# Kernel tuning notes

Hardware: AMD Instinct MI355X
Metric: run time of the kernel (lower is better)

The kernel has to match this reference:

```python
import jax, jax.numpy as jnp
import numpy as np

DEPTH = 2
DIM = 512
FF = 2048
INNER = 32
VOCAB = 8192
B = 2
L = 512
LN_EPS = 1e-5


def _layer_norm(x, g, b):
    m = jnp.mean(x, axis=-1, keepdims=True)
    v = jnp.var(x, axis=-1, keepdims=True)
    return (x - m) * jax.lax.rsqrt(v + LN_EPS) * g + b


def _sioconv_layer(x, wa, wx, v_re, v_im, h0_re, h0_im, w_ol):
    # x: [B, L, DIM] float32
    Bb, Ll, _ = x.shape
    I = v_re.shape[0]
    # complex gate a with magnitude sigmoid(log|a|^2)
    af = (x @ wa.T).reshape(Bb, Ll, I, 2)
    a = jax.lax.complex(af[..., 0], af[..., 1])
    m = jnp.square(af[..., 0]) + jnp.square(af[..., 1])
    a = a * jax.lax.rsqrt(m) * jax.nn.sigmoid(jnp.log(m))  # [B,L,I] complex
    # complex input x with magnitude |x| (x * rsqrt(|x|^2) * |x|^2)
    xf = (x @ wx.T).reshape(Bb, Ll, I, 2)
    xc = jax.lax.complex(xf[..., 0], xf[..., 1])
    mx = jnp.square(xf[..., 0]) + jnp.square(xf[..., 1])
    xc = xc * jax.lax.rsqrt(mx) * mx  # [B,L,I] complex
    # cumulative log-decay products: the original's FFT conv of the upper-
    # triangular a_ln against an all-ones matrix is exactly a cumsum along j.
    a_ln = jnp.log(a)  # [B,L,I]
    ii = jnp.arange(Ll)[:, None]
    jj = jnp.arange(Ll)[None, :]
    tri = jnp.where((jj >= ii)[None, None, :, :],
                    jnp.transpose(a_ln, (0, 2, 1))[:, :, None, :],
                    jnp.zeros((), a_ln.dtype))  # [B,I,L,L]: tri[b,d,i,j]=a_ln[b,j,d] for j>=i
    s = jnp.cumsum(tri, axis=3)
    # c[b,d,i,j] = prod_{t=i..j} a[b,t,d] for j>=i; =1 at j=i-1; 0 below.
    c = jnp.where((jj >= ii - 1)[None, None, :, :], jnp.exp(s), jnp.zeros((), s.dtype))
    V = jax.lax.complex(v_re, v_im)
    Vinv = jnp.linalg.inv(V)
    h0 = jax.lax.complex(h0_re, h0_im)  # [I]
    xct = jnp.transpose(xc, (0, 2, 1))  # [B,I,L]
    x_roll = jnp.roll(xct, 1, axis=2).at[:, :, 0].set(h0[None, :])
    # original builds C[b,l,m,n,o] = V diag(c) V^-1 then einsum; contract lazily:
    y = jnp.einsum('ko,bol->bkl', Vinv, x_roll)  # eigenbasis inputs [B,I,L]
    t = jnp.einsum('bkij,bki->bjk', c, y)        # recurrence in eigenbasis [B,L,I]
    h = jnp.einsum('bjk,nk->bjn', t, V)          # back to state basis [B,L,I]
    h = h.at[:, -1, :].add(xc[:, -1, :])         # last step input (others already in c via j=i-1 band)
    return jnp.real(h) @ w_ol.T


def setup_inputs() -> dict:
    key = jax.random.key(0)
    ks = jax.random.split(key, 16)
    f = lambda k, shp: jax.random.normal(k, shp, dtype=jnp.float32)
    return {
        'x': f(ks[0], (B, L, VOCAB)),
        'w_in': f(ks[1], (DIM, VOCAB)) * VOCAB ** -0.5,
        'b_in': jnp.zeros((DIM,), jnp.float32),
        'ln1_g': jnp.ones((DEPTH, DIM), jnp.float32),
        'ln1_b': jnp.zeros((DEPTH, DIM), jnp.float32),
        'wa': f(ks[2], (DEPTH, 2 * INNER, DIM)) * DIM ** -0.5,
        'wx': f(ks[3], (DEPTH, 2 * INNER, DIM)) * DIM ** -0.5,
        'v_re': f(ks[4], (DEPTH, INNER, INNER)),
        'v_im': f(ks[5], (DEPTH, INNER, INNER)),
        'h0_re': f(ks[6], (DEPTH, INNER)),
        'h0_im': f(ks[7], (DEPTH, INNER)),
        'w_ol': f(ks[8], (DEPTH, DIM, INNER)) * INNER ** -0.5,
        'ln2_g': jnp.ones((DEPTH, DIM), jnp.float32),
        'ln2_b': jnp.zeros((DEPTH, DIM), jnp.float32),
        'w1': f(ks[9], (DEPTH, FF, DIM)) * DIM ** -0.5,
        'b1': jnp.zeros((DEPTH, FF), jnp.float32),
        'w2': f(ks[10], (DEPTH, DIM, FF)) * FF ** -0.5,
        'b2': jnp.zeros((DEPTH, DIM), jnp.float32),
        'lnl_g': jnp.ones((DIM,), jnp.float32),
        'lnl_b': jnp.zeros((DIM,), jnp.float32),
        'w_out': f(ks[11], (VOCAB, DIM)) * DIM ** -0.5,
        'b_out': jnp.zeros((VOCAB,), jnp.float32),
    }


def reference(x, w_in, b_in, ln1_g, ln1_b, wa, wx, v_re, v_im, h0_re, h0_im,
              w_ol, ln2_g, ln2_b, w1, b1, w2, b2, lnl_g, lnl_b, w_out, b_out):
    h = x @ w_in.T + b_in  # [B,L,DIM]
    for d in range(DEPTH):
        r = h
        z = _layer_norm(h, ln1_g[d], ln1_b[d])
        z = _sioconv_layer(z, wa[d], wx[d], v_re[d], v_im[d], h0_re[d], h0_im[d], w_ol[d])
        h = z + r
        r = h
        z = _layer_norm(h, ln2_g[d], ln2_b[d])
        z = jax.nn.silu(z @ w1[d].T + b1[d]) @ w2[d].T + b2[d]
        h = z + r
    h = _layer_norm(h, lnl_g, lnl_b)
    return h @ w_out.T + b_out
```

## Files before the change

### kernel.cpp

```cpp
#include <hip/hip_runtime.h>
#include <stdint.h>

#define DEPTHC 2
#define DIMC   512
#define FFC    2048
#define INNERC 32
#define VOCABC 8192
#define BC     2
#define LC     512
#define NTOK   1024

typedef _Float16 f16;
typedef __attribute__((ext_vector_type(8))) _Float16 f16x8;
typedef __attribute__((ext_vector_type(4))) float f32x4;

__device__ __forceinline__ float2 cmul2(float2 a, float2 b){
    return make_float2(a.x*b.x - a.y*b.y, a.x*b.y + a.y*b.x);
}
__device__ __forceinline__ float2 cadd2(float2 a, float2 b){
    return make_float2(a.x + b.x, a.y + b.y);
}

__device__ __forceinline__ void gl_lds16(const void* g, void* l){
    __builtin_amdgcn_global_load_lds(
        (const __attribute__((address_space(1))) unsigned int*)g,
        (__attribute__((address_space(3))) unsigned int*)l, 16, 0, 0);
}

__global__ __launch_bounds__(256) void k_prep(
    const float* __restrict__ s0, const float* __restrict__ s1,
    const float* __restrict__ s2, const float* __restrict__ s3,
    const float* __restrict__ s4,
    const float* __restrict__ wa4, const float* __restrict__ wx4,
    f16* __restrict__ d0, f16* __restrict__ d1, f16* __restrict__ d2,
    f16* __restrict__ d3, f16* __restrict__ d4, f16* __restrict__ wgb,
    int n0, int n1, int n2, int n3, int n4,
    const float* __restrict__ v_re, const float* __restrict__ v_im,
    const float* __restrict__ h0re, const float* __restrict__ h0im,
    float2* __restrict__ vinv, float2* __restrict__ h0c)
{
    __shared__ float2 M[32][64];
    if (blockIdx.x < 2){
        const int d = blockIdx.x;
        const int tid = threadIdx.x;
        const int c = tid & 63;
        const int wv = tid >> 6;
        if (tid < 32) h0c[d*32 + tid] = make_float2(h0re[d*32 + tid], h0im[d*32 + tid]);
#pragma unroll
        for (int rr = 0; rr < 8; ++rr){
            int r = wv*8 + rr;
            float re, im;
            if (c < 32){ re = v_re[d*1024 + r*32 + c]; im = v_im[d*1024 + r*32 + c]; }
            else       { re = (c - 32 == r) ? 1.f : 0.f; im = 0.f; }
            M[r][c] = make_float2(re, im);
        }
        __syncthreads();
#pragma unroll 1
        for (int col = 0; col < 32; ++col){
            float2 prow = M[col][c];
            float pvx = __shfl(prow.x, col, 64);
            float pvy = __shfl(prow.y, col, 64);
            float dm = pvx*pvx + pvy*pvy;
            float ir = pvx/dm, ii = -pvy/dm;
            float2 nv = make_float2(prow.x*ir - prow.y*ii, prow.x*ii + prow.y*ir);
#pragma unroll
            for (int rr = 0; rr < 8; ++rr){
                int r = wv*8 + rr;
                if (r == col) continue;
                float2 f  = M[r][col];
                float2 m0 = M[r][c];
                m0.x -= f.x*nv.x - f.y*nv.y;
                m0.y -= f.x*nv.y + f.y*nv.x;
                M[r][c] = m0;
            }
            __syncthreads();
        }
        if (c >= 32){
#pragma unroll
            for (int rr = 0; rr < 8; ++rr){
                int r = wv*8 + rr;
                float2 dv = M[r][r];
                float dm = dv.x*dv.x + dv.y*dv.y;
                float ir = dv.x/dm, ii = -dv.y/dm;
                float2 m0 = M[r][c];
                vinv[d*1024 + r*32 + (c - 32)] =
                    make_float2(m0.x*ir - m0.y*ii, m0.x*ii + m0.y*ir);
            }
        }
        return;
    }
    long long i = ((long long)(blockIdx.x - 2) * 256 + threadIdx.x) * 4;
    const float* s; f16* d;
    if (i < n0){ s = s0; d = d0; }
    else { i -= n0;
        if (i < n1){ s = s1; d = d1; }
        else { i -= n1;
            if (i < n2){ s = s2; d = d2; }
            else { i -= n2;
                if (i < n3){ s = s3; d = d3; }
                else { i -= n3;
                    if (i < n4){ s = s4; d = d4; }
                    else {
                        i -= n4;
                        if (i >= 131072) return;
                        const float* gs; f16* gd;
                        if (i < 65536){
                            int dd = (int)(i >> 15), rem = (int)(i & 32767);
                            gs = wa4 + i; gd = wgb + dd*65536 + rem;
                        } else {
                            long long e2 = i - 65536;
                            int dd = (int)(e2 >> 15), rem = (int)(e2 & 32767);
                            gs = wx4 + e2; gd = wgb + dd*65536 + 32768 + rem;
                        }
                        float4 v = *(const float4*)gs;
                        union { f16 h[4]; float2 f2; } u;
                        u.h[0] = (f16)v.x; u.h[1] = (f16)v.y; u.h[2] = (f16)v.z; u.h[3] = (f16)v.w;
                        *(float2*)gd = u.f2;
                        return;
                    }
                }
            }
        }
    }
    float4 v = *(const float4*)(s + i);
    union { f16 h[4]; float2 f2; } u;
    u.h[0] = (f16)v.x; u.h[1] = (f16)v.y; u.h[2] = (f16)v.z; u.h[3] = (f16)v.w;
    *(float2*)(d + i) = u.f2;
}

template<int MT, int NT, int MODE>
__global__ __launch_bounds__(256) void k_gemmT(
    const f16* __restrict__ A, const f16* __restrict__ Bw,
    void* __restrict__ C, const float* __restrict__ bias,
    int N, int K, int klen, int partStride,
    float2* __restrict__ a_tp, float2* __restrict__ xcp)
{
    constexpr int RM = MT/32, RN = NT/32;
    __shared__ __align__(16) f16 As[MT*64];
    __shared__ __align__(16) f16 Bs[NT*64];
    const int tid = threadIdx.x;
    const int m0 = blockIdx.y * MT;
    const int n0 = blockIdx.x * NT;
    const int kbeg = blockIdx.z * klen;
    const int l = tid & 63;
    const int w = tid >> 6;
    const int fr = l & 15;
    const int fq = l >> 4;
    const int wm = (w >> 1) * (MT/2);
    const int wn = (w & 1) * (NT/2);
    const f16* gA = A  + (size_t)(m0 + (tid >> 3)) * K + kbeg + (tid & 7) * 8;
    const f16* gB = Bw + (size_t)(n0 + (tid >> 3)) * K + kbeg + (tid & 7) * 8;
    const size_t rowskip = (size_t)32 * K;
    f16* lA = As + tid * 8;
    f16* lB = Bs + tid * 8;
    f32x4 acc[RM][RN];
#pragma unroll
    for (int i = 0; i < RM; ++i)
#pragma unroll
        for (int j = 0; j < RN; ++j)
            acc[i][j] = (f32x4){0.f, 0.f, 0.f, 0.f};
    for (int kk = 0; kk < klen; kk += 64){
        __syncthreads();
#pragma unroll
        for (int i = 0; i < MT/32; ++i) gl_lds16(gA + i*rowskip, lA + i*2048);
#pragma unroll
        for (int i = 0; i < NT/32; ++i) gl_lds16(gB + i*rowskip, lB + i*2048);
        gA += 64; gB += 64;
        __syncthreads();
#pragma unroll
        for (int h = 0; h < 2; ++h){
            f16x8 af[RM], bf[RN];
#pragma unroll
            for (int i = 0; i < RM; ++i) af[i] = *(const f16x8*)(As + (wm + 16*i + fr) * 64 + h*32 + fq * 8);
#pragma unroll
            for (int j = 0; j < RN; ++j) bf[j] = *(const f16x8*)(Bs + (wn + 16*j + fr) * 64 + h*32 + fq * 8);
#pragma unroll
            for (int i = 0; i < RM; ++i)
#pragma unroll
                for (int j = 0; j < RN; ++j)
                    acc[i][j] = __builtin_amdgcn_mfma_f32_16x16x32_f16(af[i], bf[j], acc[i][j], 0, 0, 0);
        }
    }
#pragma unroll
    for (int i = 0; i < RM; ++i)
#pragma unroll
        for (int j = 0; j < RN; ++j)
#pragma unroll
            for (int r = 0; r < 4; ++r){
                int row = m0 + wm + 16*i + fq*4 + r;
                int col = n0 + wn + 16*j + fr;
                if (MODE == 1){
                    ((f16*)C + (size_t)blockIdx.z * partStride)[(size_t)row * N + col] = (f16)acc[i][j][r];
                } else if (MODE == 0){
                    ((float*)C)[(size_t)row * N + col] = acc[i][j][r] + bias[col];
                } else if (MODE == 2){
                    float v = acc[i][j][r] + bias[col];
                    ((f16*)C)[(size_t)row * N + col] = (f16)(v / (1.f + __expf(-v)));
                } else {
                    float val = acc[i][j][r];
                    float pv = __shfl_xor(val, 1, 64);
                    if (!(fr & 1)){
                        float re = val, im = pv;
                        int bb = row >> 9, t = row & 511;
                        float m2 = re*re + im*im;
                        if (col < 64){
                            int k = col >> 1;
                            float sa = rsqrtf(m2) * (m2 / (1.f + m2));
                            a_tp[(size_t)(bb*INNERC + k)*LC + t] = make_float2(re*sa, im*sa);
                        } else {
                            int k = (col - 64) >> 1;
                            float sx = sqrtf(m2);
                            xcp[(size_t)row*INNERC + k] = make_float2(re*sx, im*sx);
                        }
                    }
                }
            }
}

__global__ __launch_bounds__(128) void k_ln1(
    const f16* __restrict__ part, const float* __restrict__ bias,
    const float* __restrict__ res, const float* __restrict__ g,
    const float* __restrict__ b, f16* __restrict__ out,
    float* __restrict__ hout, int n)
{
    int row = blockIdx.x;
    int tid = threadIdx.x;
    __shared__ float sw[2], qw[2];
    float v[4]; float s = 0.f, q = 0.f;
#pragma unroll
    for (int j = 0; j < 4; ++j){
        int c = tid + 128*j;
        int idx = row*DIMC + c;
        float t = bias[c];
        if (res) t += res[idx];
#pragma unroll
        for (int z = 0; z < 8; ++z) t += (float)part[(size_t)z * n + idx];
        if (hout) hout[idx] = t;
        v[j] = t; s += t; q += t*t;
    }
    for (int off = 32; off; off >>= 1){ s += __shfl_down(s, off, 64); q += __shfl_down(q, off, 64); }
    if ((tid & 63) == 0){ sw[tid >> 6] = s; qw[tid >> 6] = q; }
    __syncthreads();
    float S = sw[0] + sw[1], Q = qw[0] + qw[1];
    float m = S / DIMC;
    float rstd = rsqrtf(Q / DIMC - m*m + 1e-5f);
#pragma unroll
    for (int j = 0; j < 4; ++j){
        int c = tid + 128*j;
        out[(size_t)row*DIMC + c] = (f16)((v[j] - m)*rstd*g[c] + b[c]);
    }
}

__global__ __launch_bounds__(64) void k_scan(
    const float2* __restrict__ a_t, const float2* __restrict__ xc,
    const float2* __restrict__ vinv, const float2* __restrict__ h0c,
    float2* __restrict__ e)
{
    int bk = blockIdx.x;
    int l = threadIdx.x;
    int bb = bk >> 5, k = bk & 31;
    float2 vrow[32];
#pragma unroll
    for (int o = 0; o < 32; ++o) vrow[o] = vinv[k*32 + o];
    int base = bk * LC + l * 8;
    float2 av[8], wv[8];
#pragma unroll
    for (int j = 0; j < 8; ++j) av[j] = a_t[base + j];
#pragma unroll
    for (int j = 0; j < 8; ++j){
        int t = l*8 + j;
        const float2* src = (t == 0) ? h0c : (xc + (size_t)(bb*LC + t - 1) * INNERC);
        float2 acc = make_float2(0.f, 0.f);
#pragma unroll
        for (int o = 0; o < 32; o += 2){
            float4 qq = *(const float4*)(src + o);
            acc.x += vrow[o].x*qq.x - vrow[o].y*qq.y;
            acc.y += vrow[o].x*qq.y + vrow[o].y*qq.x;
            acc.x += vrow[o+1].x*qq.z - vrow[o+1].y*qq.w;
            acc.y += vrow[o+1].x*qq.w + vrow[o+1].y*qq.z;
        }
        wv[j] = acc;
    }
    float2 A = make_float2(1.f, 0.f), Bc = make_float2(0.f, 0.f);
#pragma unroll
    for (int j = 0; j < 8; ++j){
        Bc = cmul2(av[j], cadd2(Bc, wv[j]));
        A  = cmul2(av[j], A);
    }
    for (int off = 1; off < 64; off <<= 1){
        float Apx = __shfl_up(A.x,  off, 64), Apy = __shfl_up(A.y,  off, 64);
        float Bpx = __shfl_up(Bc.x, off, 64), Bpy = __shfl_up(Bc.y, off, 64);
        if (l >= off){
            float2 Ap = make_float2(Apx, Apy), Bp = make_float2(Bpx, Bpy);
            Bc = cadd2(cmul2(A, Bp), Bc);
            A  = cmul2(A, Ap);
        }
    }
    float ex = __shfl_up(Bc.x, 1, 64), ey = __shfl_up(Bc.y, 1, 64);
    float2 ecur = (l == 0) ? make_float2(0.f, 0.f) : make_float2(ex, ey);
    size_t obase = ((size_t)bb*LC + l*8) * INNERC + k;
#pragma unroll
    for (int j = 0; j < 8; ++j){
        ecur = cmul2(av[j], cadd2(ecur, wv[j]));
        e[obase + (size_t)j * INNERC] = ecur;
    }
}

__global__ __launch_bounds__(128) void k_siout_ln(
    const float2* __restrict__ e, const float2* __restrict__ xc,
    const float* __restrict__ vre, const float* __restrict__ vim,
    const float* __restrict__ wol, const float* __restrict__ res,
    const float* __restrict__ g2, const float* __restrict__ b2,
    float* __restrict__ hout, f16* __restrict__ zout)
{
    int bt = blockIdx.x;
    int tid = threadIdx.x;
    __shared__ float hr[INNERC];
    __shared__ float2 er[INNERC];
    __shared__ float sw[2], qw[2];
    if (tid < 32) er[tid] = e[(size_t)bt*INNERC + tid];
    __syncthreads();
    if (tid < 32){
        const float* vrr = vre + tid*INNERC;
        const float* vir = vim + tid*INNERC;
        float acc = xc[(size_t)bt*INNERC + tid].x;
#pragma unroll
        for (int k2 = 0; k2 < 32; ++k2) acc += vrr[k2]*er[k2].x - vir[k2]*er[k2].y;
        hr[tid] = acc;
    }
    __syncthreads();
    float v[4]; float s = 0.f, q = 0.f;
#pragma unroll
    for (int j = 0; j < 4; ++j){
        int n = tid + 128*j;
        float val = res[(size_t)bt*DIMC + n];
        const float* wr = wol + (size_t)n * INNERC;
#pragma unroll
        for (int i = 0; i < 32; ++i) val += hr[i]*wr[i];
        hout[(size_t)bt*DIMC + n] = val;
        v[j] = val; s += val; q += val*val;
    }
    for (int off = 32; off; off >>= 1){ s += __shfl_down(s, off, 64); q += __shfl_down(q, off, 64); }
    if ((tid & 63) == 0){ sw[tid >> 6] = s; qw[tid >> 6] = q; }
    __syncthreads();
    float S = sw[0] + sw[1], Q = qw[0] + qw[1];
    float m = S / DIMC;
    float rstd = rsqrtf(Q / DIMC - m*m + 1e-5f);
#pragma unroll
    for (int j = 0; j < 4; ++j){
        int n = tid + 128*j;
        zout[(size_t)bt*DIMC + n] = (f16)((v[j] - m)*rstd*g2[n] + b2[n]);
    }
}

extern "C" void kernel_launch(void* const* d_in, const int* in_sizes, int n_in,
                              void* d_out, int out_size, void* d_ws, size_t ws_size,
                              hipStream_t stream)
{
    const float* x     = (const float*)d_in[0];
    const float* w_in  = (const float*)d_in[1];
    const float* b_in  = (const float*)d_in[2];
    const float* ln1_g = (const float*)d_in[3];
    const float* ln1_b = (const float*)d_in[4];
    const float* wa    = (const float*)d_in[5];
    const float* wx    = (const float*)d_in[6];
    const float* v_re  = (const float*)d_in[7];
    const float* v_im  = (const float*)d_in[8];
    const float* h0_re = (const float*)d_in[9];
    const float* h0_im = (const float*)d_in[10];
    const float* w_ol  = (const float*)d_in[11];
    const float* ln2_g = (const float*)d_in[12];
    const float* ln2_b = (const float*)d_in[13];
    const float* w1    = (const float*)d_in[14];
    const float* b1    = (const float*)d_in[15];
    const float* w2    = (const float*)d_in[16];
    const float* b2    = (const float*)d_in[17];
    const float* lnl_g = (const float*)d_in[18];
    const float* lnl_b = (const float*)d_in[19];
    const float* w_out = (const float*)d_in[20];
    const float* b_out = (const float*)d_in[21];

    char* p = (char*)d_ws;
    f16* xb   = (f16*)p;   p += (size_t)NTOK * VOCABC * 2;
    f16* wib  = (f16*)p;   p += (size_t)DIMC * VOCABC * 2;
    f16* wob  = (f16*)p;   p += (size_t)VOCABC * DIMC * 2;
    f16* w1b  = (f16*)p;   p += (size_t)DEPTHC * FFC * DIMC * 2;
    f16* w2b  = (f16*)p;   p += (size_t)DEPTHC * DIMC * FFC * 2;
    f16* wgb  = (f16*)p;   p += (size_t)DEPTHC * 2*INNERC*2 * DIMC * 2;
    float* h1 = (float*)p; p += (size_t)NTOK * DIMC * 4;
    float* h2 = (float*)p; p += (size_t)NTOK * DIMC * 4;
    float* h3 = (float*)p; p += (size_t)NTOK * DIMC * 4;
    f16* zb   = (f16*)p;   p += (size_t)NTOK * DIMC * 2;
    f16* ffb  = (f16*)p;   p += (size_t)NTOK * FFC * 2;
    f16* pbuf = (f16*)p;   p += (size_t)8 * NTOK * DIMC * 2;
    float2* a_t = (float2*)p; p += (size_t)BC * INNERC * LC * 8;
    float2* xc  = (float2*)p; p += (size_t)NTOK * INNERC * 8;
    float2* ev  = (float2*)p; p += (size_t)NTOK * INNERC * 8;
    float2* vinv = (float2*)p; p += (size_t)DEPTHC * INNERC * INNERC * 8;
    float2* h0c  = (float2*)p; p += (size_t)DEPTHC * INNERC * 8;

    {
        const int n0 = NTOK*VOCABC, n1 = DIMC*VOCABC, n2 = DEPTHC*FFC*DIMC,
                  n3 = DEPTHC*DIMC*FFC, n4 = VOCABC*DIMC;
        int blocks = (n0 + n1 + n2 + n3 + n4 + 131072) / 1024 + 2;
        k_prep<<<blocks, 256, 0, stream>>>(x, w_in, w1, w2, w_out, wa, wx,
                                           xb, wib, w1b, w2b, wob, wgb,
                                           n0, n1, n2, n3, n4,
                                           v_re, v_im, h0_re, h0_im, vinv, h0c);
    }

    {
        dim3 g(DIMC/128, NTOK/64, 8);
        k_gemmT<64,128,1><<<g, 256, 0, stream>>>(xb, wib, pbuf, nullptr, DIMC, VOCABC, VOCABC/8, NTOK*DIMC,
                                                 nullptr, nullptr);
    }

    for (int d = 0; d < DEPTHC; ++d){
        float* cur = (d == 0) ? h1 : h3;
        float* hb  = h2;
        const float* redBias = (d == 0) ? b_in : (b2 + (d-1)*DIMC);
        const float* redRes  = (d == 0) ? nullptr : h2;
        k_ln1<<<NTOK, 128, 0, stream>>>(pbuf, redBias, redRes,
                                        ln1_g + d*DIMC, ln1_b + d*DIMC, zb, cur, NTOK*DIMC);
        {
            dim3 g(1, NTOK/32, 1);
            k_gemmT<32,128,3><<<g, 256, 0, stream>>>(zb, wgb + (size_t)d*128*DIMC, nullptr, nullptr,
                                                     128, DIMC, DIMC, 0, a_t, xc);
        }
        k_scan<<<BC*INNERC, 64, 0, stream>>>(a_t, xc, vinv + d*INNERC*INNERC, h0c + d*INNERC, ev);
        k_siout_ln<<<NTOK, 128, 0, stream>>>(ev, xc, v_re + d*INNERC*INNERC, v_im + d*INNERC*INNERC,
                                             w_ol + (size_t)d*DIMC*INNERC, cur,
                                             ln2_g + d*DIMC, ln2_b + d*DIMC, hb, zb);
        {
            dim3 g(FFC/128, NTOK/64, 1);
            k_gemmT<64,128,2><<<g, 256, 0, stream>>>(zb, w1b + (size_t)d*FFC*DIMC, ffb, b1 + d*FFC,
                                                     FFC, DIMC, DIMC, 0, nullptr, nullptr);
        }
        {
            dim3 g(DIMC/128, NTOK/64, 8);
            k_gemmT<64,128,1><<<g, 256, 0, stream>>>(ffb, w2b + (size_t)d*DIMC*FFC, pbuf, nullptr,
                                                     DIMC, FFC, FFC/8, NTOK*DIMC, nullptr, nullptr);
        }
    }
    k_ln1<<<NTOK, 128, 0, stream>>>(pbuf, b2 + (DEPTHC-1)*DIMC, h2, lnl_g, lnl_b, zb, nullptr, NTOK*DIMC);
    {
        dim3 g(VOCABC/128, NTOK/128, 1);
        k_gemmT<128,128,0><<<g, 256, 0, stream>>>(zb, wob, (float*)d_out, b_out, VOCABC, DIMC, DIMC, 0,
                                                  nullptr, nullptr);
    }
    (void)in_sizes; (void)n_in; (void)out_size; (void)ws_size;
}
```

Before: 337.3 us.

## XOR-swizzle GEMM shared-memory tiles and widen fp16 conversion to 8 elements

The GEMM tile loader now XOR-permutes each row's 16-byte chunk index by the row index when staging A and B into shared memory. The fragment reads apply the same permutation, so the MFMA operand loads from rows spaced 64 halves apart fall in different LDS banks instead of conflicting. Separately, the fp32-to-fp16 prep kernel now converts 8 elements per thread with two float4 loads and one 16-byte store, which halves the launched block count and widens the stores. The swizzle depends on the row offsets staying multiples of 8, which holds for the current tile shapes.

```diff
diff --git a/kernel.cpp b/kernel.cpp
--- a/kernel.cpp
+++ b/kernel.cpp
@@ -89,7 +89,7 @@
         }
         return;
     }
-    long long i = ((long long)(blockIdx.x - 2) * 256 + threadIdx.x) * 4;
+    long long i = ((long long)(blockIdx.x - 2) * 256 + threadIdx.x) * 8;
     const float* s; f16* d;
     if (i < n0){ s = s0; d = d0; }
     else { i -= n0;
@@ -112,20 +112,24 @@
                             int dd = (int)(e2 >> 15), rem = (int)(e2 & 32767);
                             gs = wx4 + e2; gd = wgb + dd*65536 + 32768 + rem;
                         }
-                        float4 v = *(const float4*)gs;
-                        union { f16 h[4]; float2 f2; } u;
-                        u.h[0] = (f16)v.x; u.h[1] = (f16)v.y; u.h[2] = (f16)v.z; u.h[3] = (f16)v.w;
-                        *(float2*)gd = u.f2;
+                        float4 va = *(const float4*)gs;
+                        float4 vb = *(const float4*)(gs + 4);
+                        union { f16 h[8]; float4 f4; } u;
+                        u.h[0] = (f16)va.x; u.h[1] = (f16)va.y; u.h[2] = (f16)va.z; u.h[3] = (f16)va.w;
+                        u.h[4] = (f16)vb.x; u.h[5] = (f16)vb.y; u.h[6] = (f16)vb.z; u.h[7] = (f16)vb.w;
+                        *(float4*)gd = u.f4;
                         return;
                     }
                 }
             }
         }
     }
-    float4 v = *(const float4*)(s + i);
-    union { f16 h[4]; float2 f2; } u;
-    u.h[0] = (f16)v.x; u.h[1] = (f16)v.y; u.h[2] = (f16)v.z; u.h[3] = (f16)v.w;
-    *(float2*)(d + i) = u.f2;
+    float4 va = *(const float4*)(s + i);
+    float4 vb = *(const float4*)(s + i + 4);
+    union { f16 h[8]; float4 f4; } u;
+    u.h[0] = (f16)va.x; u.h[1] = (f16)va.y; u.h[2] = (f16)va.z; u.h[3] = (f16)va.w;
+    u.h[4] = (f16)vb.x; u.h[5] = (f16)vb.y; u.h[6] = (f16)vb.z; u.h[7] = (f16)vb.w;
+    *(float4*)(d + i) = u.f4;
 }
 
 template<int MT, int NT, int MODE>
@@ -146,10 +150,13 @@
     const int w = tid >> 6;
     const int fr = l & 15;
     const int fq = l >> 4;
+    const int kx = l & 7;
     const int wm = (w >> 1) * (MT/2);
     const int wn = (w & 1) * (NT/2);
-    const f16* gA = A  + (size_t)(m0 + (tid >> 3)) * K + kbeg + (tid & 7) * 8;
-    const f16* gB = Bw + (size_t)(n0 + (tid >> 3)) * K + kbeg + (tid & 7) * 8;
+    const int srow = tid >> 3;
+    const int schunk = (tid & 7) ^ (srow & 7);
+    const f16* gA = A  + (size_t)(m0 + srow) * K + kbeg + schunk * 8;
+    const f16* gB = Bw + (size_t)(n0 + srow) * K + kbeg + schunk * 8;
     const size_t rowskip = (size_t)32 * K;
     f16* lA = As + tid * 8;
     f16* lB = Bs + tid * 8;
@@ -171,9 +178,11 @@
         for (int h = 0; h < 2; ++h){
             f16x8 af[RM], bf[RN];
 #pragma unroll
-            for (int i = 0; i < RM; ++i) af[i] = *(const f16x8*)(As + (wm + 16*i + fr) * 64 + h*32 + fq * 8);
-#pragma unroll
-            for (int j = 0; j < RN; ++j) bf[j] = *(const f16x8*)(Bs + (wn + 16*j + fr) * 64 + h*32 + fq * 8);
+            for (int i = 0; i < RM; ++i)
+                af[i] = *(const f16x8*)(As + (wm + 16*i + fr) * 64 + (((h*4 + fq) ^ kx)) * 8);
+#pragma unroll
+            for (int j = 0; j < RN; ++j)
+                bf[j] = *(const f16x8*)(Bs + (wn + 16*j + fr) * 64 + (((h*4 + fq) ^ kx)) * 8);
 #pragma unroll
             for (int i = 0; i < RM; ++i)
 #pragma unroll
@@ -402,7 +411,7 @@
     {
         const int n0 = NTOK*VOCABC, n1 = DIMC*VOCABC, n2 = DEPTHC*FFC*DIMC,
                   n3 = DEPTHC*DIMC*FFC, n4 = VOCABC*DIMC;
-        int blocks = (n0 + n1 + n2 + n3 + n4 + 131072) / 1024 + 2;
+        int blocks = (n0 + n1 + n2 + n3 + n4 + 131072) / 2048 + 2;
         k_prep<<<blocks, 256, 0, stream>>>(x, w_in, w1, w2, w_out, wa, wx,
                                            xb, wib, w1b, w2b, wob, wgb,
                                            n0, n1, n2, n3, n4,
```

Result: faster. 329.4 us (-2.3%).
